# Kernel optimization log

Hardware: AMD Instinct MI355X
Metric: run time of the kernel (lower is better)

The kernel has to match this reference:

```python
import jax, jax.numpy as jnp
import numpy as np

B, S, D, H = 16, 512, 1024, 16
DH = D // H  # 64


def setup_inputs() -> dict:
    key = jax.random.key(0)
    kx, kq, kk, kv = jax.random.split(key, 4)
    stdv = 1.0 / np.sqrt(DH)  # reset_param uses 1/sqrt(t.size(1)) = 1/sqrt(head_dim)
    x = jax.random.normal(kx, (B, S, D), dtype=jnp.float32)
    Wq = jax.random.uniform(kq, (H, D, DH), dtype=jnp.float32, minval=-stdv, maxval=stdv)
    Wk = jax.random.uniform(kk, (H, D, DH), dtype=jnp.float32, minval=-stdv, maxval=stdv)
    Wv = jax.random.uniform(kv, (H, D, DH), dtype=jnp.float32, minval=-stdv, maxval=stdv)
    return {"x": x, "Wq": Wq, "Wk": Wk, "Wv": Wv}


def reference(x, Wq, Wk, Wv):
    # x: [B, S, D]; Wq/Wk/Wv: [H, D, DH] (stacked per-head params)
    q = jnp.einsum('bsd,hde->bhse', x, Wq)  # [B,H,S,DH]
    k = jnp.einsum('bsd,hde->bhse', x, Wk)
    v = jnp.einsum('bsd,hde->bhse', x, Wv)
    # NOTE: original scales by sqrt(input_dim), not sqrt(head_dim)
    scale = 1.0 / jnp.sqrt(jnp.float32(D))
    scores = jnp.einsum('bhse,bhte->bhst', q, k) * scale  # [B,H,S,S]
    attn = jax.nn.softmax(scores, axis=-1)
    out = jnp.einsum('bhst,bhte->bhse', attn, v)  # [B,H,S,DH]
    # concat heads along feature dim (head order matches torch cat over loop)
    return out.transpose(0, 2, 1, 3).reshape(x.shape[0], x.shape[1], D)
```

## Files before the change

kernel.cpp:

```cpp
#include <hip/hip_runtime.h>
#include <math.h>

constexpr int B = 16, S = 512, D = 1024, H = 16, DH = 64;
constexpr int BH = B * H;

typedef short bf16x8 __attribute__((ext_vector_type(8)));
typedef float f32x4  __attribute__((ext_vector_type(4)));

__device__ __forceinline__ unsigned short f2bf(float f) {
    unsigned u = __float_as_uint(f);
    u += 0x7fff + ((u >> 16) & 1);
    return (unsigned short)(u >> 16);
}

#define VMC0  asm volatile("s_waitcnt vmcnt(0)" ::: "memory")
#define LGKM0 asm volatile("s_waitcnt lgkmcnt(0)" ::: "memory")
#define BARR  __builtin_amdgcn_s_barrier()

__global__ __launch_bounds__(256) void convert_all(
    const float* __restrict__ x, unsigned short* __restrict__ xb,
    const float* __restrict__ Wq, const float* __restrict__ Wk,
    const float* __restrict__ Wv, unsigned short* __restrict__ WbT)
{
    __shared__ float tile[64][65];
    const int t = threadIdx.x;
    const int bx = blockIdx.x;

    if (bx < 8192) {
        int i = bx * 256 + t;
        float4 v = ((const float4*)x)[i];
        ushort4 o;
        o.x = f2bf(v.x); o.y = f2bf(v.y); o.z = f2bf(v.z); o.w = f2bf(v.w);
        ((ushort4*)xb)[i] = o;
        return;
    }

    const int cw = bx - 8192;
    const int d0 = (cw & 15) * 64;
    const int h = (cw >> 4) & 15;
    const int m = cw >> 8;
    const float* W = ((m == 0) ? Wq : (m == 1) ? Wk : Wv) + (size_t)h * D * DH;
    {
        int e = t & 63, dr = t >> 6;
        #pragma unroll
        for (int i = 0; i < 16; ++i) {
            int d = dr * 16 + i;
            tile[d][e] = W[(size_t)(d0 + d) * DH + e];
        }
    }
    __syncthreads();
    {
        int d = t & 63, er = t >> 6;
        unsigned short* out = WbT + (size_t)(m * H + h) * DH * D;
        #pragma unroll
        for (int i = 0; i < 16; ++i) {
            int e = er * 16 + i;
            out[(size_t)e * D + d0 + d] = f2bf(tile[d][e]);
        }
    }
}

__global__ __launch_bounds__(256) void qkv_gemm(
    const unsigned short* __restrict__ xb,
    const unsigned short* __restrict__ WbT,
    unsigned short* __restrict__ qkvb)
{
    __shared__ unsigned short As[128 * 64];
    __shared__ unsigned short Bs[128 * 64];

    const int t = threadIdx.x;
    const int w = t >> 6;
    const int wr = w >> 1, wc = w & 1;
    const int L = t & 63;
    const int lane15 = L & 15;
    const int quad = L >> 4;
    const int lrow8 = L >> 3;
    const int lg = L & 7;

    const int r0 = blockIdx.x * 128;
    const int n0 = blockIdx.y * 128;

    f32x4 acc[4][4] = {};

    for (int k0 = 0; k0 < D; k0 += 64) {
        #pragma unroll
        for (int i = 0; i < 4; ++i) {
            int c = w * 4 + i;
            int r = c * 8 + lrow8;
            int gg = lg ^ (r & 7);
            const unsigned short* gp = xb + (size_t)(r0 + r) * D + k0 + gg * 8;
            __builtin_amdgcn_global_load_lds(
                (const __attribute__((address_space(1))) void*)gp,
                (__attribute__((address_space(3))) void*)(As + c * 512),
                16, 0, 0);
            const unsigned short* gq = WbT + (size_t)(n0 + r) * D + k0 + gg * 8;
            __builtin_amdgcn_global_load_lds(
                (const __attribute__((address_space(1))) void*)gq,
                (__attribute__((address_space(3))) void*)(Bs + c * 512),
                16, 0, 0);
        }
        __syncthreads();

        #pragma unroll
        for (int ks = 0; ks < 2; ++ks) {
            int gk = ks * 4 + quad;
            bf16x8 a[4], bb[4];
            #pragma unroll
            for (int rt = 0; rt < 4; ++rt) {
                int ml = wr * 64 + rt * 16 + lane15;
                a[rt] = *(const bf16x8*)(As + ml * 64 + ((gk ^ (ml & 7)) * 8));
            }
            #pragma unroll
            for (int ct = 0; ct < 4; ++ct) {
                int nl = wc * 64 + ct * 16 + lane15;
                bb[ct] = *(const bf16x8*)(Bs + nl * 64 + ((gk ^ (nl & 7)) * 8));
            }
            #pragma unroll
            for (int rt = 0; rt < 4; ++rt)
                #pragma unroll
                for (int ct = 0; ct < 4; ++ct)
                    acc[rt][ct] = __builtin_amdgcn_mfma_f32_16x16x32_bf16(
                        a[rt], bb[ct], acc[rt][ct], 0, 0, 0);
        }
        __syncthreads();
    }

    const int m  = n0 >> 10;
    const int h  = ((n0 >> 6) + wc) & 15;
    const int bb_ = r0 >> 9;
    const int s0 = (r0 & 511) + wr * 64;

    if (m == 2) {
        unsigned short* outv = qkvb + ((size_t)(2 * BH) + (bb_ * H + h)) * (size_t)(S * DH);
        #pragma unroll
        for (int rt = 0; rt < 4; ++rt) {
            int srow = s0 + rt * 16 + quad * 4;
            #pragma unroll
            for (int ct = 0; ct < 4; ++ct) {
                int e = ct * 16 + lane15;
                ushort4 pk;
                pk.x = f2bf(acc[rt][ct][0]);
                pk.y = f2bf(acc[rt][ct][1]);
                pk.z = f2bf(acc[rt][ct][2]);
                pk.w = f2bf(acc[rt][ct][3]);
                *(ushort4*)(outv + (size_t)e * S + srow) = pk;
            }
        }
    } else {
        const float sc = (m == 0) ? 0.04508422002778011f : 1.0f;
        unsigned short* out = qkvb + ((size_t)m * BH + (bb_ * H + h)) * (size_t)(S * DH);
        #pragma unroll
        for (int rt = 0; rt < 4; ++rt) {
            #pragma unroll
            for (int ct = 0; ct < 4; ++ct) {
                int e = ct * 16 + lane15;
                #pragma unroll
                for (int r = 0; r < 4; ++r) {
                    int srow = s0 + rt * 16 + quad * 4 + r;
                    out[(size_t)srow * DH + e] = f2bf(acc[rt][ct][r] * sc);
                }
            }
        }
    }
}

__global__ __launch_bounds__(512, 4) void attn_mfma(
    const unsigned short* __restrict__ qkvb, float* __restrict__ out)
{
    __shared__ unsigned short KV[2][2][64 * 64];
    unsigned short* Qs = &KV[0][0][0];

    const int t = threadIdx.x;
    const int w = t >> 6;
    const int L = t & 63;
    const int lane15 = L & 15;
    const int quad = L >> 4;
    const int lrow8 = L >> 3;
    const int lg = L & 7;
    const int qr0 = blockIdx.x * 128;
    const int bh = blockIdx.y;
    const int b = bh >> 4, h = bh & 15;

    const unsigned short* qb = qkvb + (size_t)bh * S * DH;
    const unsigned short* kb = qkvb + (size_t)(BH + bh) * S * DH;
    const unsigned short* vt = qkvb + (size_t)(2 * BH + bh) * S * DH;

    #pragma unroll
    for (int p = 0; p < 2; ++p) {
        int base = p * 64 + w * 8;
        int r = base + lrow8;
        int gg = lg ^ (r & 7);
        __builtin_amdgcn_global_load_lds(
            (const __attribute__((address_space(1))) void*)
                (qb + (size_t)(qr0 + r) * DH + gg * 8),
            (__attribute__((address_space(3))) void*)(Qs + base * 64),
            16, 0, 0);
    }
    VMC0;
    BARR;

    bf16x8 qf[2];
    #pragma unroll
    for (int ks = 0; ks < 2; ++ks) {
        int ml = w * 16 + lane15;
        int gk = ks * 4 + quad;
        qf[ks] = *(const bf16x8*)(Qs + ml * 64 + ((gk ^ (lane15 & 7)) * 8));
    }
    LGKM0;
    BARR;

    {
        int r = w * 8 + lrow8;
        int gr = (r & 32) | ((r & 12) << 1) | ((r & 16) >> 2) | (r & 3);
        int gg = lg ^ (r & 7);
        __builtin_amdgcn_global_load_lds(
            (const __attribute__((address_space(1))) void*)
                (kb + (size_t)gr * DH + gg * 8),
            (__attribute__((address_space(3))) void*)(&KV[0][0][0] + (w * 8) * 64),
            16, 0, 0);
        __builtin_amdgcn_global_load_lds(
            (const __attribute__((address_space(1))) void*)
                (vt + (size_t)r * S + gg * 8),
            (__attribute__((address_space(3))) void*)(&KV[0][1][0] + (w * 8) * 64),
            16, 0, 0);
    }
    VMC0;
    BARR;

    f32x4 o[4] = {};
    float plsum = 0.f;

    #pragma unroll 2
    for (int kt = 0; kt < 8; ++kt) {
        const int cur = kt & 1;
        const unsigned short* Kt  = &KV[cur][0][0];
        const unsigned short* Vtl = &KV[cur][1][0];

        f32x4 st[4] = {};
        #pragma unroll
        for (int ks = 0; ks < 2; ++ks) {
            int gk = ks * 4 + quad;
            bf16x8 kf[4];
            #pragma unroll
            for (int ct = 0; ct < 4; ++ct) {
                int kr = ct * 16 + lane15;
                kf[ct] = *(const bf16x8*)(Kt + kr * 64 + ((gk ^ (lane15 & 7)) * 8));
            }
            __builtin_amdgcn_s_setprio(1);
            #pragma unroll
            for (int ct = 0; ct < 4; ++ct)
                st[ct] = __builtin_amdgcn_mfma_f32_16x16x32_bf16(
                    kf[ct], qf[ks], st[ct], 0, 0, 0);
            __builtin_amdgcn_s_setprio(0);
        }

        bf16x8 pB[2];
        {
            float rs = 0.f;
            union { unsigned u[4]; bf16x8 v; } pu[2];
            #pragma unroll
            for (int ct = 0; ct < 4; ++ct) {
                float p0 = exp2f(st[ct][0]);
                float p1 = exp2f(st[ct][1]);
                float p2 = exp2f(st[ct][2]);
                float p3 = exp2f(st[ct][3]);
                rs += (p0 + p1) + (p2 + p3);
                unsigned lo, hi;
                asm("v_cvt_pk_bf16_f32 %0, %1, %2" : "=v"(lo) : "v"(p0), "v"(p1));
                asm("v_cvt_pk_bf16_f32 %0, %1, %2" : "=v"(hi) : "v"(p2), "v"(p3));
                pu[ct >> 1].u[(ct & 1) * 2 + 0] = lo;
                pu[ct >> 1].u[(ct & 1) * 2 + 1] = hi;
            }
            pB[0] = pu[0].v;
            pB[1] = pu[1].v;
            plsum += rs;
        }

        #pragma unroll
        for (int ks = 0; ks < 2; ++ks) {
            int gk = ks * 4 + quad;
            bf16x8 vf[4];
            #pragma unroll
            for (int nt = 0; nt < 4; ++nt) {
                int dh = nt * 16 + lane15;
                vf[nt] = *(const bf16x8*)(Vtl + dh * 64 + ((gk ^ (lane15 & 7)) * 8));
            }
            __builtin_amdgcn_s_setprio(1);
            #pragma unroll
            for (int nt = 0; nt < 4; ++nt)
                o[nt] = __builtin_amdgcn_mfma_f32_16x16x32_bf16(
                    vf[nt], pB[ks], o[nt], 0, 0, 0);
            __builtin_amdgcn_s_setprio(0);
        }

        if (kt < 7) {
            int r = w * 8 + lrow8;
            int gr = (r & 32) | ((r & 12) << 1) | ((r & 16) >> 2) | (r & 3);
            int gg = lg ^ (r & 7);
            int kn = (kt + 1) * 64;
            __builtin_amdgcn_global_load_lds(
                (const __attribute__((address_space(1))) void*)
                    (kb + (size_t)(kn + gr) * DH + gg * 8),
                (__attribute__((address_space(3))) void*)(&KV[cur ^ 1][0][0] + (w * 8) * 64),
                16, 0, 0);
            __builtin_amdgcn_global_load_lds(
                (const __attribute__((address_space(1))) void*)
                    (vt + (size_t)r * S + kn + gg * 8),
                (__attribute__((address_space(3))) void*)(&KV[cur ^ 1][1][0] + (w * 8) * 64),
                16, 0, 0);
            VMC0;
            BARR;
        }
    }

    {
        float l = plsum;
        l += __shfl_xor(l, 16, 64);
        l += __shfl_xor(l, 32, 64);
        float inv = 1.0f / l;
        int srow = qr0 + w * 16 + lane15;
        float* op = out + (size_t)(b * S + srow) * D + h * DH;
        #pragma unroll
        for (int nt = 0; nt < 4; ++nt) {
            float4 v;
            v.x = o[nt][0] * inv;
            v.y = o[nt][1] * inv;
            v.z = o[nt][2] * inv;
            v.w = o[nt][3] * inv;
            *(float4*)(op + nt * 16 + quad * 4) = v;
        }
    }
}

extern "C" void kernel_launch(void* const* d_in, const int* in_sizes, int n_in,
                              void* d_out, int out_size, void* d_ws, size_t ws_size,
                              hipStream_t stream) {
    const float* x  = (const float*)d_in[0];
    const float* Wq = (const float*)d_in[1];
    const float* Wk = (const float*)d_in[2];
    const float* Wv = (const float*)d_in[3];
    float* outp = (float*)d_out;

    unsigned short* qkvb = (unsigned short*)d_ws;
    unsigned short* xb   = (unsigned short*)((char*)d_ws + 50331648);
    unsigned short* WbT  = (unsigned short*)((char*)d_ws + 67108864);

    convert_all<<<dim3(8192 + 768), 256, 0, stream>>>(x, xb, Wq, Wk, Wv, WbT);
    qkv_gemm<<<dim3(B * S / 128, 3 * H * DH / 128), 256, 0, stream>>>(xb, WbT, qkvb);
    attn_mfma<<<dim3(S / 128, BH), 512, 0, stream>>>(qkvb, outp);
}
```

Baseline: 193.0 us.

## Use 32x32x16 MFMA in QKV GEMM and split launch into Q/K and V parts

The QKV projection GEMM switches from 16x16x32 to 32x32x16 bf16 MFMA tiles, so each wave holds 2x2 accumulators of 16 floats and issues fewer LDS fragment loads per MFMA. The epilogue index math is rewritten for the 32x32 output layout. The single GEMM launch is also split into two launches (Q/K columns, then V columns) using an n_base offset. This adds a second launch and changes register pressure, in exchange for higher MFMA efficiency and less LDS traffic.

```diff
diff --git a/kernel.cpp b/kernel.cpp
--- a/kernel.cpp
+++ b/kernel.cpp
@@ -6,6 +6,7 @@
 
 typedef short bf16x8 __attribute__((ext_vector_type(8)));
 typedef float f32x4  __attribute__((ext_vector_type(4)));
+typedef float f32x16 __attribute__((ext_vector_type(16)));
 
 __device__ __forceinline__ unsigned short f2bf(float f) {
     unsigned u = __float_as_uint(f);
@@ -63,7 +64,7 @@
 __global__ __launch_bounds__(256) void qkv_gemm(
     const unsigned short* __restrict__ xb,
     const unsigned short* __restrict__ WbT,
-    unsigned short* __restrict__ qkvb)
+    unsigned short* __restrict__ qkvb, int n_base)
 {
     __shared__ unsigned short As[128 * 64];
     __shared__ unsigned short Bs[128 * 64];
@@ -72,15 +73,15 @@
     const int w = t >> 6;
     const int wr = w >> 1, wc = w & 1;
     const int L = t & 63;
-    const int lane15 = L & 15;
-    const int quad = L >> 4;
+    const int lane31 = L & 31;
+    const int hi = L >> 5;
     const int lrow8 = L >> 3;
     const int lg = L & 7;
 
     const int r0 = blockIdx.x * 128;
-    const int n0 = blockIdx.y * 128;
-
-    f32x4 acc[4][4] = {};
+    const int n0 = n_base + blockIdx.y * 128;
+
+    f32x16 acc[2][2] = {};
 
     for (int k0 = 0; k0 < D; k0 += 64) {
         #pragma unroll
@@ -102,24 +103,24 @@
         __syncthreads();
 
         #pragma unroll
-        for (int ks = 0; ks < 2; ++ks) {
-            int gk = ks * 4 + quad;
-            bf16x8 a[4], bb[4];
-            #pragma unroll
-            for (int rt = 0; rt < 4; ++rt) {
-                int ml = wr * 64 + rt * 16 + lane15;
-                a[rt] = *(const bf16x8*)(As + ml * 64 + ((gk ^ (ml & 7)) * 8));
-            }
-            #pragma unroll
-            for (int ct = 0; ct < 4; ++ct) {
-                int nl = wc * 64 + ct * 16 + lane15;
-                bb[ct] = *(const bf16x8*)(Bs + nl * 64 + ((gk ^ (nl & 7)) * 8));
-            }
-            #pragma unroll
-            for (int rt = 0; rt < 4; ++rt)
+        for (int ks4 = 0; ks4 < 4; ++ks4) {
+            int g = ks4 * 2 + hi;
+            bf16x8 a[2], bb[2];
+            #pragma unroll
+            for (int rt = 0; rt < 2; ++rt) {
+                int ml = wr * 64 + rt * 32 + lane31;
+                a[rt] = *(const bf16x8*)(As + ml * 64 + ((g ^ (ml & 7)) * 8));
+            }
+            #pragma unroll
+            for (int ct = 0; ct < 2; ++ct) {
+                int nl = wc * 64 + ct * 32 + lane31;
+                bb[ct] = *(const bf16x8*)(Bs + nl * 64 + ((g ^ (nl & 7)) * 8));
+            }
+            #pragma unroll
+            for (int rt = 0; rt < 2; ++rt)
                 #pragma unroll
-                for (int ct = 0; ct < 4; ++ct)
-                    acc[rt][ct] = __builtin_amdgcn_mfma_f32_16x16x32_bf16(
+                for (int ct = 0; ct < 2; ++ct)
+                    acc[rt][ct] = __builtin_amdgcn_mfma_f32_32x32x16_bf16(
                         a[rt], bb[ct], acc[rt][ct], 0, 0, 0);
         }
         __syncthreads();
@@ -133,34 +134,35 @@
     if (m == 2) {
         unsigned short* outv = qkvb + ((size_t)(2 * BH) + (bb_ * H + h)) * (size_t)(S * DH);
         #pragma unroll
-        for (int rt = 0; rt < 4; ++rt) {
-            int srow = s0 + rt * 16 + quad * 4;
-            #pragma unroll
-            for (int ct = 0; ct < 4; ++ct) {
-                int e = ct * 16 + lane15;
-                ushort4 pk;
-                pk.x = f2bf(acc[rt][ct][0]);
-                pk.y = f2bf(acc[rt][ct][1]);
-                pk.z = f2bf(acc[rt][ct][2]);
-                pk.w = f2bf(acc[rt][ct][3]);
-                *(ushort4*)(outv + (size_t)e * S + srow) = pk;
-            }
-        }
+        for (int rt = 0; rt < 2; ++rt)
+            #pragma unroll
+            for (int ct = 0; ct < 2; ++ct) {
+                int e = ct * 32 + lane31;
+                #pragma unroll
+                for (int rg = 0; rg < 4; ++rg) {
+                    int srow = s0 + rt * 32 + rg * 8 + hi * 4;
+                    ushort4 pk;
+                    pk.x = f2bf(acc[rt][ct][rg * 4 + 0]);
+                    pk.y = f2bf(acc[rt][ct][rg * 4 + 1]);
+                    pk.z = f2bf(acc[rt][ct][rg * 4 + 2]);
+                    pk.w = f2bf(acc[rt][ct][rg * 4 + 3]);
+                    *(ushort4*)(outv + (size_t)e * S + srow) = pk;
+                }
+            }
     } else {
         const float sc = (m == 0) ? 0.04508422002778011f : 1.0f;
         unsigned short* out = qkvb + ((size_t)m * BH + (bb_ * H + h)) * (size_t)(S * DH);
         #pragma unroll
-        for (int rt = 0; rt < 4; ++rt) {
-            #pragma unroll
-            for (int ct = 0; ct < 4; ++ct) {
-                int e = ct * 16 + lane15;
+        for (int rt = 0; rt < 2; ++rt)
+            #pragma unroll
+            for (int ct = 0; ct < 2; ++ct) {
+                int e = ct * 32 + lane31;
                 #pragma unroll
-                for (int r = 0; r < 4; ++r) {
-                    int srow = s0 + rt * 16 + quad * 4 + r;
+                for (int r = 0; r < 16; ++r) {
+                    int srow = s0 + rt * 32 + (r & 3) + 8 * (r >> 2) + 4 * hi;
                     out[(size_t)srow * DH + e] = f2bf(acc[rt][ct][r] * sc);
                 }
             }
-        }
     }
 }
 
@@ -346,6 +348,7 @@
     unsigned short* WbT  = (unsigned short*)((char*)d_ws + 67108864);
 
     convert_all<<<dim3(8192 + 768), 256, 0, stream>>>(x, xb, Wq, Wk, Wv, WbT);
-    qkv_gemm<<<dim3(B * S / 128, 3 * H * DH / 128), 256, 0, stream>>>(xb, WbT, qkvb);
+    qkv_gemm<<<dim3(B * S / 128, 16), 256, 0, stream>>>(xb, WbT, qkvb, 0);
+    qkv_gemm<<<dim3(B * S / 128, 8),  256, 0, stream>>>(xb, WbT, qkvb, 2048);
     attn_mfma<<<dim3(S / 128, BH), 512, 0, stream>>>(qkvb, outp);
 }
```

Measured after the change: 197.3 us. 1.02x slower.

## Double-buffer LDS tiles in QKV GEMM to overlap global loads with MFMA

Applied to the files above, without the earlier changes.

The QKV projection GEMM now keeps two LDS buffers for A and B tiles. The next K-slice is prefetched with global_load_lds while MFMAs run on the current slice, which replaces the load-then-sync-then-compute serialization. Fragments are read into registers before the prefetch is issued, and s_setprio raises wave priority around the MFMA block. This doubles the LDS footprint to 64 KB per block, which may reduce occupancy, and adds register pressure from holding both k-substeps of fragments.

```diff
diff --git a/kernel.cpp b/kernel.cpp
--- a/kernel.cpp
+++ b/kernel.cpp
@@ -60,13 +60,37 @@
     }
 }
 
+__device__ __forceinline__ void qkv_stage(
+    const unsigned short* __restrict__ xb,
+    const unsigned short* __restrict__ WbT,
+    unsigned short* Ad, unsigned short* Bd,
+    int r0, int n0, int k0, int w, int lrow8, int lg)
+{
+    #pragma unroll
+    for (int i = 0; i < 4; ++i) {
+        int c = w * 4 + i;
+        int r = c * 8 + lrow8;
+        int gg = lg ^ (r & 7);
+        __builtin_amdgcn_global_load_lds(
+            (const __attribute__((address_space(1))) void*)
+                (xb + (size_t)(r0 + r) * D + k0 + gg * 8),
+            (__attribute__((address_space(3))) void*)(Ad + c * 512),
+            16, 0, 0);
+        __builtin_amdgcn_global_load_lds(
+            (const __attribute__((address_space(1))) void*)
+                (WbT + (size_t)(n0 + r) * D + k0 + gg * 8),
+            (__attribute__((address_space(3))) void*)(Bd + c * 512),
+            16, 0, 0);
+    }
+}
+
 __global__ __launch_bounds__(256) void qkv_gemm(
     const unsigned short* __restrict__ xb,
     const unsigned short* __restrict__ WbT,
     unsigned short* __restrict__ qkvb)
 {
-    __shared__ unsigned short As[128 * 64];
-    __shared__ unsigned short Bs[128 * 64];
+    __shared__ unsigned short As[2][128 * 64];
+    __shared__ unsigned short Bs[2][128 * 64];
 
     const int t = threadIdx.x;
     const int w = t >> 6;
@@ -82,47 +106,48 @@
 
     f32x4 acc[4][4] = {};
 
-    for (int k0 = 0; k0 < D; k0 += 64) {
-        #pragma unroll
-        for (int i = 0; i < 4; ++i) {
-            int c = w * 4 + i;
-            int r = c * 8 + lrow8;
-            int gg = lg ^ (r & 7);
-            const unsigned short* gp = xb + (size_t)(r0 + r) * D + k0 + gg * 8;
-            __builtin_amdgcn_global_load_lds(
-                (const __attribute__((address_space(1))) void*)gp,
-                (__attribute__((address_space(3))) void*)(As + c * 512),
-                16, 0, 0);
-            const unsigned short* gq = WbT + (size_t)(n0 + r) * D + k0 + gg * 8;
-            __builtin_amdgcn_global_load_lds(
-                (const __attribute__((address_space(1))) void*)gq,
-                (__attribute__((address_space(3))) void*)(Bs + c * 512),
-                16, 0, 0);
-        }
-        __syncthreads();
-
+    qkv_stage(xb, WbT, &As[0][0], &Bs[0][0], r0, n0, 0, w, lrow8, lg);
+    VMC0;
+    BARR;
+
+    #pragma unroll 2
+    for (int kt = 0; kt < 16; ++kt) {
+        const int cur = kt & 1;
+
+        bf16x8 a[2][4], bb[2][4];
         #pragma unroll
         for (int ks = 0; ks < 2; ++ks) {
             int gk = ks * 4 + quad;
-            bf16x8 a[4], bb[4];
             #pragma unroll
             for (int rt = 0; rt < 4; ++rt) {
                 int ml = wr * 64 + rt * 16 + lane15;
-                a[rt] = *(const bf16x8*)(As + ml * 64 + ((gk ^ (ml & 7)) * 8));
+                a[ks][rt] = *(const bf16x8*)(&As[cur][0] + ml * 64 + ((gk ^ (ml & 7)) * 8));
             }
             #pragma unroll
             for (int ct = 0; ct < 4; ++ct) {
                 int nl = wc * 64 + ct * 16 + lane15;
-                bb[ct] = *(const bf16x8*)(Bs + nl * 64 + ((gk ^ (nl & 7)) * 8));
-            }
+                bb[ks][ct] = *(const bf16x8*)(&Bs[cur][0] + nl * 64 + ((gk ^ (nl & 7)) * 8));
+            }
+        }
+        __builtin_amdgcn_sched_barrier(0);
+
+        if (kt < 15)
+            qkv_stage(xb, WbT, &As[cur ^ 1][0], &Bs[cur ^ 1][0],
+                      r0, n0, (kt + 1) * 64, w, lrow8, lg);
+
+        __builtin_amdgcn_s_setprio(1);
+        #pragma unroll
+        for (int ks = 0; ks < 2; ++ks)
             #pragma unroll
             for (int rt = 0; rt < 4; ++rt)
                 #pragma unroll
                 for (int ct = 0; ct < 4; ++ct)
                     acc[rt][ct] = __builtin_amdgcn_mfma_f32_16x16x32_bf16(
-                        a[rt], bb[ct], acc[rt][ct], 0, 0, 0);
-        }
-        __syncthreads();
+                        a[ks][rt], bb[ks][ct], acc[rt][ct], 0, 0, 0);
+        __builtin_amdgcn_s_setprio(0);
+
+        VMC0;
+        BARR;
     }
 
     const int m  = n0 >> 10;
```

Measured after the change: 180.4 us. 6.5% less time.
